# Kernel optimization log

Hardware: AMD Instinct MI355X
Metric: run time of the kernel (lower is better)

Reference implementation:

```python
import jax, jax.numpy as jnp
import numpy as np

DIM = 768
DEPTH = 6
HEADS = 12
DIM_HEAD = 64
INNER = HEADS * DIM_HEAD  # 768
MLP = DIM * 4
B, N = 4, 2048
EPS = 1e-5


def setup_inputs() -> dict:
    key = jax.random.key(0)
    ks = jax.random.split(key, 8)
    s = lambda *sh: 0.02
    inp = {
        "x": jax.random.normal(ks[0], (B, N, DIM), dtype=jnp.float32),
        "ln1_g": jnp.ones((DEPTH, DIM), jnp.float32),
        "ln1_b": jnp.zeros((DEPTH, DIM), jnp.float32),
        "wqkv": jax.random.normal(ks[1], (DEPTH, DIM, 3 * INNER), jnp.float32) * 0.02,
        "wout": jax.random.normal(ks[2], (DEPTH, INNER, DIM), jnp.float32) * 0.02,
        "ln2_g": jnp.ones((DEPTH, DIM), jnp.float32),
        "ln2_b": jnp.zeros((DEPTH, DIM), jnp.float32),
        "w1": jax.random.normal(ks[3], (DEPTH, DIM, MLP), jnp.float32) * 0.02,
        "b1": jnp.zeros((DEPTH, MLP), jnp.float32),
        "w2": jax.random.normal(ks[4], (DEPTH, MLP, DIM), jnp.float32) * 0.02,
        "b2": jnp.zeros((DEPTH, DIM), jnp.float32),
        "fn_g": jnp.ones((DIM,), jnp.float32),
        "fn_b": jnp.zeros((DIM,), jnp.float32),
    }
    return inp


def layer_norm(x, g, b):
    mu = jnp.mean(x, axis=-1, keepdims=True)
    var = jnp.mean(jnp.square(x - mu), axis=-1, keepdims=True)
    return (x - mu) * jax.lax.rsqrt(var + EPS) * g + b


def attention(x, wqkv, wout):
    # x: [b, n, dim]
    qkv = x @ wqkv  # [b, n, 3*inner]
    q, k, v = jnp.split(qkv, 3, axis=-1)
    split_heads = lambda t: t.reshape(t.shape[0], t.shape[1], HEADS, DIM_HEAD).transpose(0, 2, 1, 3)
    q, k, v = split_heads(q), split_heads(k), split_heads(v)  # [b, h, n, d]
    scale = DIM_HEAD ** -0.5
    dots = jnp.einsum("bhnd,bhmd->bhnm", q, k) * scale
    attn = jax.nn.softmax(dots, axis=-1)
    out = jnp.einsum("bhnm,bhmd->bhnd", attn, v)
    out = out.transpose(0, 2, 1, 3).reshape(x.shape[0], x.shape[1], INNER)
    return out @ wout


def feed_forward(x, w1, b1, w2, b2):
    h = jax.nn.gelu(x @ w1 + b1, approximate=False)
    return h @ w2 + b2


def reference(x, ln1_g, ln1_b, wqkv, wout, ln2_g, ln2_b, w1, b1, w2, b2, fn_g, fn_b):
    for i in range(DEPTH):
        x = x + attention(layer_norm(x, ln1_g[i], ln1_b[i]), wqkv[i], wout[i])
        x = x + feed_forward(layer_norm(x, ln2_g[i], ln2_b[i]), w1[i], b1[i], w2[i], b2[i])
    return layer_norm(x, fn_g, fn_b)
```

## Files before the change

### kernel.cpp

```cpp
#include <hip/hip_runtime.h>
#include <hip/hip_bf16.h>

typedef unsigned short ushort_t;
typedef unsigned int uint_t;
typedef __bf16 bf16x8 __attribute__((ext_vector_type(8)));
typedef float floatx4 __attribute__((ext_vector_type(4)));
typedef float floatx16 __attribute__((ext_vector_type(16)));

#define DIM 768
#define DEPTH 6
#define HEADS 12
#define DH 64
#define MLP_DIM 3072
#define BATCH 4
#define SEQ 2048
#define MTOK (BATCH * SEQ)
#define QKV3 (3 * DIM)

__device__ __forceinline__ float bf2f(unsigned u) {
    return __uint_as_float((u & 0xffffu) << 16);
}
__device__ __forceinline__ ushort_t f2bf(float f) {
    unsigned x = __float_as_uint(f);
    return (ushort_t)((x + 0x7FFFu + ((x >> 16) & 1u)) >> 16);
}
__device__ __forceinline__ void load_lds16(const void* g, void* l) {
    __builtin_amdgcn_global_load_lds((const __attribute__((address_space(1))) uint_t*)g,
                                     (__attribute__((address_space(3))) uint_t*)l, 16, 0, 0);
}
__device__ __forceinline__ uint_t cvt_pk_bf16(float lo, float hi) {
    uint_t r;
    asm("v_cvt_pk_bf16_f32 %0, %1, %2" : "=v"(r) : "v"(lo), "v"(hi));
    return r;
}
__device__ __forceinline__ float exp2_raw(float x) {
#if __has_builtin(__builtin_amdgcn_exp2f)
    return __builtin_amdgcn_exp2f(x);
#else
    return exp2f(x);
#endif
}

__global__ __launch_bounds__(256) void transpose_cvt(const float* __restrict__ in,
                                                     ushort_t* __restrict__ out,
                                                     int K, int N) {
    __shared__ float tile[32][33];
    const int d = blockIdx.z;
    in += (size_t)d * K * N;
    out += (size_t)d * K * N;
    const int n0 = blockIdx.x * 32, k0 = blockIdx.y * 32;
    for (int i = threadIdx.y; i < 32; i += 8) {
        tile[i][threadIdx.x] = in[(size_t)(k0 + i) * N + n0 + threadIdx.x];
    }
    __syncthreads();
    for (int i = threadIdx.y; i < 32; i += 8) {
        out[(size_t)(n0 + i) * K + k0 + threadIdx.x] = f2bf(tile[threadIdx.x][i]);
    }
}

template <bool OUTBF>
__global__ __launch_bounds__(256) void layernorm_k(const float* __restrict__ x,
                                                   const float* __restrict__ g,
                                                   const float* __restrict__ bta,
                                                   void* __restrict__ out) {
    const int row = blockIdx.x, t = threadIdx.x;
    const float* xr = x + (size_t)row * DIM;
    float v0 = xr[t], v1 = xr[t + 256], v2 = xr[t + 512];
    float s = v0 + v1 + v2;
    float sq = v0 * v0 + v1 * v1 + v2 * v2;
#pragma unroll
    for (int off = 32; off > 0; off >>= 1) {
        s += __shfl_down(s, off, 64);
        sq += __shfl_down(sq, off, 64);
    }
    __shared__ float ss[4], ssq[4];
    const int w = t >> 6;
    if ((t & 63) == 0) { ss[w] = s; ssq[w] = sq; }
    __syncthreads();
    s = ss[0] + ss[1] + ss[2] + ss[3];
    sq = ssq[0] + ssq[1] + ssq[2] + ssq[3];
    const float mean = s * (1.0f / DIM);
    const float var = sq * (1.0f / DIM) - mean * mean;
    const float rstd = rsqrtf(var + 1e-5f);
    float y0 = (v0 - mean) * rstd * g[t] + bta[t];
    float y1 = (v1 - mean) * rstd * g[t + 256] + bta[t + 256];
    float y2 = (v2 - mean) * rstd * g[t + 512] + bta[t + 512];
    if (OUTBF) {
        ushort_t* o = (ushort_t*)out + (size_t)row * DIM;
        o[t] = f2bf(y0); o[t + 256] = f2bf(y1); o[t + 512] = f2bf(y2);
    } else {
        float* o = (float*)out + (size_t)row * DIM;
        o[t] = y0; o[t + 256] = y1; o[t + 512] = y2;
    }
}

template <bool BIAS, bool GELU, bool RES, bool OUTBF>
__global__ __launch_bounds__(256) void gemm_bt(const ushort_t* __restrict__ A,
                                               const ushort_t* __restrict__ Bt,
                                               const float* __restrict__ bias,
                                               const float* __restrict__ resid,
                                               void* __restrict__ Cout,
                                               int M, int N, int K) {
    __shared__ ushort_t lds_a[2][128 * 32];
    __shared__ ushort_t lds_b[2][128 * 32];
    const int t = threadIdx.x;
    const int lane = t & 63, w = t >> 6;
    const int wm = w >> 1, wn = w & 1;

    const int nwg = gridDim.x * gridDim.y;
    int bid = blockIdx.y * gridDim.x + blockIdx.x;
    bid = (bid & 7) * (nwg >> 3) + (bid >> 3);
    const int bx = bid % gridDim.x, by = bid / gridDim.x;
    const int bm = by * 128, bn = bx * 128;

    floatx4 acc[4][4];
#pragma unroll
    for (int i = 0; i < 4; i++)
#pragma unroll
        for (int j = 0; j < 4; j++) acc[i][j] = (floatx4)0.0f;

    const int arow = t >> 2;
    const int asw = ((t & 3) ^ ((t >> 3) & 3)) * 8;
    const ushort_t* Abase = A + (size_t)(bm + arow) * K + asw;
    const ushort_t* Bbase = Bt + (size_t)(bn + arow) * K + asw;

    const int mrow = wm * 64 + (lane & 15);
    const int nrow = wn * 64 + (lane & 15);
    const int quad = lane >> 4;
    const int kca = (quad ^ ((mrow >> 1) & 3)) * 8;
    const int kcb = (quad ^ ((nrow >> 1) & 3)) * 8;

    const int nk = K >> 5;
    auto stage = [&](int kt) {
        const int bsel = kt & 1;
        const int k0 = kt * 32;
        ushort_t* la = lds_a[bsel] + t * 8;
        ushort_t* lb = lds_b[bsel] + t * 8;
        load_lds16(Abase + k0, la);
        load_lds16(Abase + (size_t)64 * K + k0, la + 64 * 32);
        load_lds16(Bbase + k0, lb);
        load_lds16(Bbase + (size_t)64 * K + k0, lb + 64 * 32);
    };

    stage(0);
    for (int kt = 0; kt < nk; kt++) {
        __syncthreads();
        if (kt + 1 < nk) stage(kt + 1);
        const ushort_t* la = lds_a[kt & 1];
        const ushort_t* lb = lds_b[kt & 1];

        bf16x8 af[4], bfr[4];
#pragma unroll
        for (int i = 0; i < 4; i++) {
            af[i] = *(const bf16x8*)(la + (mrow + i * 16) * 32 + kca);
            bfr[i] = *(const bf16x8*)(lb + (nrow + i * 16) * 32 + kcb);
        }
#pragma unroll
        for (int i = 0; i < 4; i++)
#pragma unroll
            for (int j = 0; j < 4; j++)
                acc[i][j] = __builtin_amdgcn_mfma_f32_16x16x32_bf16(af[i], bfr[j], acc[i][j], 0, 0, 0);
    }

    const int colq = lane & 15, rq = lane >> 4;
#pragma unroll
    for (int j = 0; j < 4; j++) {
        const int col = bn + wn * 64 + j * 16 + colq;
        const float bv = BIAS ? bias[col] : 0.0f;
#pragma unroll
        for (int i = 0; i < 4; i++) {
#pragma unroll
            for (int r = 0; r < 4; r++) {
                const int row = bm + wm * 64 + i * 16 + rq * 4 + r;
                float v = acc[i][j][r] + bv;
                if (GELU) v = 0.5f * v * (1.0f + erff(v * 0.70710678118654752f));
                const size_t idx = (size_t)row * N + col;
                if (RES) v += resid[idx];
                if (OUTBF) ((ushort_t*)Cout)[idx] = f2bf(v);
                else ((float*)Cout)[idx] = v;
            }
        }
    }
}

#define TSTR 66

__global__ __launch_bounds__(256) void v_transpose(const ushort_t* __restrict__ qkv,
                                                   ushort_t* __restrict__ vt) {
    __shared__ ushort_t tile[64 * TSTR];
    const int t = threadIdx.x;
    const int tk = blockIdx.x, h = blockIdx.y, b = blockIdx.z;
#pragma unroll
    for (int rep = 0; rep < 2; rep++) {
        const int s = t + rep * 256;
        const int row = s >> 3, uo = (s & 7) * 8;
        *(uint4*)(tile + row * TSTR + uo) =
            *(const uint4*)(qkv + (size_t)(b * SEQ + tk * 64 + row) * QKV3 + 2 * DIM + h * DH + uo);
    }
    __syncthreads();
#pragma unroll
    for (int rep = 0; rep < 2; rep++) {
        const int s = t + rep * 256;
        const int d = s >> 3, to = (s & 7) * 8;
        ushort_t tmp[8];
#pragma unroll
        for (int j = 0; j < 8; j++) tmp[j] = tile[(to + j) * TSTR + d];
        *(uint4*)(vt + ((size_t)(b * HEADS + h) * DH + d) * SEQ + tk * 64 + to) = *(uint4*)tmp;
    }
}

#define SC2 0.18033688011112042f

__global__ __launch_bounds__(256, 3) void attn_mfma(const ushort_t* __restrict__ qkv,
                                                    const ushort_t* __restrict__ vt,
                                                    ushort_t* __restrict__ outp) {
    __shared__ ushort_t lds_k[2][64 * 64];
    __shared__ ushort_t lds_vt[2][64 * 64];

    const int t = threadIdx.x;
    const int lane = t & 63, w = t >> 6;
    const int h = blockIdx.y, b = blockIdx.z;
    const int q0 = blockIdx.x * 128 + w * 32;
    const int l31 = lane & 31, hi = lane >> 5;

    bf16x8 qf[4];
#pragma unroll
    for (int dc = 0; dc < 4; dc++) {
        const uint4 raw = *(const uint4*)(qkv + (size_t)(b * SEQ + q0 + l31) * QKV3 +
                                          h * DH + dc * 16 + hi * 8);
        const uint_t rr[4] = {raw.x, raw.y, raw.z, raw.w};
        union { ushort_t u[8]; bf16x8 v; } qq;
#pragma unroll
        for (int e = 0; e < 4; e++) {
            qq.u[2 * e] = f2bf(bf2f(rr[e]) * SC2);
            qq.u[2 * e + 1] = f2bf(bf2f(rr[e] >> 16) * SC2);
        }
        qf[dc] = qq.v;
    }

    union { ushort_t u[8]; bf16x8 v; } onef;
#pragma unroll
    for (int e = 0; e < 8; e++) onef.u[e] = 0x3F80;

    floatx16 o[2];
    o[0] = (floatx16)0.0f; o[1] = (floatx16)0.0f;
    floatx16 osum = (floatx16)0.0f;

    const int srow = w * 16 + (lane >> 3);
    const int sg = ((lane & 7) ^ ((lane >> 3) & 7)) * 8;
    const ushort_t* kgbase = qkv + (size_t)(b * SEQ + srow) * QKV3 + DIM + h * DH + sg;
    const ushort_t* vgbase = vt + ((size_t)(b * HEADS + h) * DH + srow) * SEQ + sg;

    auto stage = [&](int kt) {
        const int bsel = kt & 1;
        ushort_t* ldk = (ushort_t*)lds_k[bsel] + w * 16 * 64;
        ushort_t* ldv = (ushort_t*)lds_vt[bsel] + w * 16 * 64;
        const ushort_t* kg = kgbase + (size_t)kt * 64 * QKV3;
        const ushort_t* vg = vgbase + kt * 64;
        load_lds16(kg, ldk);
        load_lds16(kg + (size_t)8 * QKV3, ldk + 8 * 64);
        load_lds16(vg, ldv);
        load_lds16(vg + (size_t)8 * SEQ, ldv + 8 * 64);
    };

    stage(0);
    for (int kt = 0; kt < SEQ / 64; kt++) {
        __syncthreads();
        stage((kt + 1) & (SEQ / 64 - 1));
        const ushort_t* ldk = lds_k[kt & 1];
        const ushort_t* ldv = lds_vt[kt & 1];

#pragma unroll
        for (int kt2 = 0; kt2 < 2; kt2++) {
            const int krow = kt2 * 32 + l31;
            const int ksw = krow & 7;
            floatx16 s = (floatx16)0.0f;
#pragma unroll
            for (int dc = 0; dc < 4; dc++) {
                const bf16x8 kf = *(const bf16x8*)(ldk + krow * 64 + ((dc * 2 + hi) ^ ksw) * 8);
                s = __builtin_amdgcn_mfma_f32_32x32x16_bf16(kf, qf[dc], s, 0, 0, 0);
            }

            bf16x8 vfr[2][2];
#pragma unroll
            for (int kc = 0; kc < 2; kc++)
#pragma unroll
                for (int dhalf = 0; dhalf < 2; dhalf++) {
                    const int vrow = dhalf * 32 + l31;
                    const int kcg = kt2 * 2 + kc;
                    vfr[kc][dhalf] =
                        *(const bf16x8*)(ldv + vrow * 64 + (((kcg * 2 + hi) ^ (vrow & 7)) * 8));
                }

            float p[16];
#pragma unroll
            for (int r = 0; r < 16; r++) p[r] = exp2_raw(s[r]);

#pragma unroll
            for (int kc = 0; kc < 2; kc++) {
                uint_t da = cvt_pk_bf16(p[kc * 8 + 0], p[kc * 8 + 1]);
                uint_t db = cvt_pk_bf16(p[kc * 8 + 2], p[kc * 8 + 3]);
                uint_t dcq = cvt_pk_bf16(p[kc * 8 + 4], p[kc * 8 + 5]);
                uint_t dd = cvt_pk_bf16(p[kc * 8 + 6], p[kc * 8 + 7]);
                asm volatile("v_permlane32_swap_b32 %0, %1" : "+v"(da), "+v"(dcq));
                asm volatile("v_permlane32_swap_b32 %0, %1" : "+v"(db), "+v"(dd));
                union { uint_t u[4]; bf16x8 v; } pa;
                pa.u[0] = da; pa.u[1] = db; pa.u[2] = dcq; pa.u[3] = dd;
                osum = __builtin_amdgcn_mfma_f32_32x32x16_bf16(pa.v, onef.v, osum, 0, 0, 0);
                o[0] = __builtin_amdgcn_mfma_f32_32x32x16_bf16(pa.v, vfr[kc][0], o[0], 0, 0, 0);
                o[1] = __builtin_amdgcn_mfma_f32_32x32x16_bf16(pa.v, vfr[kc][1], o[1], 0, 0, 0);
            }
        }
    }

#pragma unroll
    for (int r = 0; r < 16; r++) {
        const int ql = (r & 3) + 8 * (r >> 2) + 4 * hi;
        const float inv = 1.0f / osum[r];
        const size_t rowbase = (size_t)(b * SEQ + q0 + ql) * DIM + h * DH;
        outp[rowbase + l31] = f2bf(o[0][r] * inv);
        outp[rowbase + 32 + l31] = f2bf(o[1][r] * inv);
    }
}

extern "C" void kernel_launch(void* const* d_in, const int* in_sizes, int n_in,
                              void* d_out, int out_size, void* d_ws, size_t ws_size,
                              hipStream_t stream) {
    const float* x_in  = (const float*)d_in[0];
    const float* ln1_g = (const float*)d_in[1];
    const float* ln1_b = (const float*)d_in[2];
    const float* wqkv  = (const float*)d_in[3];
    const float* wout  = (const float*)d_in[4];
    const float* ln2_g = (const float*)d_in[5];
    const float* ln2_b = (const float*)d_in[6];
    const float* w1    = (const float*)d_in[7];
    const float* b1    = (const float*)d_in[8];
    const float* w2    = (const float*)d_in[9];
    const float* b2    = (const float*)d_in[10];
    const float* fn_g  = (const float*)d_in[11];
    const float* fn_b  = (const float*)d_in[12];

    char* ws = (char*)d_ws;
    size_t off = 0;
    auto alloc = [&](size_t bytes) -> char* {
        char* p = ws + off;
        off = (off + bytes + 255) & ~(size_t)255;
        return p;
    };
    ushort_t* wT_qkv = (ushort_t*)alloc((size_t)DEPTH * QKV3 * DIM * 2);
    ushort_t* wT_out = (ushort_t*)alloc((size_t)DEPTH * DIM * DIM * 2);
    ushort_t* wT_1   = (ushort_t*)alloc((size_t)DEPTH * MLP_DIM * DIM * 2);
    ushort_t* wT_2   = (ushort_t*)alloc((size_t)DEPTH * DIM * MLP_DIM * 2);
    float*    xbuf   = (float*)alloc((size_t)MTOK * DIM * 4);
    ushort_t* lnbuf  = (ushort_t*)alloc((size_t)MTOK * DIM * 2);
    ushort_t* qkvbuf = (ushort_t*)alloc((size_t)MTOK * QKV3 * 2);
    ushort_t* attnbuf= (ushort_t*)alloc((size_t)MTOK * DIM * 2);
    ushort_t* hbuf   = (ushort_t*)alloc((size_t)MTOK * MLP_DIM * 2);
    ushort_t* vtbuf  = hbuf;
    (void)ws_size; (void)in_sizes; (void)n_in; (void)out_size;

    transpose_cvt<<<dim3(QKV3 / 32, DIM / 32, DEPTH), dim3(32, 8), 0, stream>>>(wqkv, wT_qkv, DIM, QKV3);
    transpose_cvt<<<dim3(DIM / 32, DIM / 32, DEPTH), dim3(32, 8), 0, stream>>>(wout, wT_out, DIM, DIM);
    transpose_cvt<<<dim3(MLP_DIM / 32, DIM / 32, DEPTH), dim3(32, 8), 0, stream>>>(w1, wT_1, DIM, MLP_DIM);
    transpose_cvt<<<dim3(DIM / 32, MLP_DIM / 32, DEPTH), dim3(32, 8), 0, stream>>>(w2, wT_2, MLP_DIM, DIM);

    hipMemcpyAsync(xbuf, x_in, (size_t)MTOK * DIM * sizeof(float), hipMemcpyDeviceToDevice, stream);

    for (int i = 0; i < DEPTH; i++) {
        layernorm_k<true><<<MTOK, 256, 0, stream>>>(xbuf, ln1_g + i * DIM, ln1_b + i * DIM, lnbuf);
        gemm_bt<false, false, false, true><<<dim3(QKV3 / 128, MTOK / 128), 256, 0, stream>>>(
            lnbuf, wT_qkv + (size_t)i * QKV3 * DIM, nullptr, nullptr, qkvbuf, MTOK, QKV3, DIM);
        v_transpose<<<dim3(SEQ / 64, HEADS, BATCH), 256, 0, stream>>>(qkvbuf, vtbuf);
        attn_mfma<<<dim3(SEQ / 128, HEADS, BATCH), 256, 0, stream>>>(qkvbuf, vtbuf, attnbuf);
        gemm_bt<false, false, true, false><<<dim3(DIM / 128, MTOK / 128), 256, 0, stream>>>(
            attnbuf, wT_out + (size_t)i * DIM * DIM, nullptr, xbuf, xbuf, MTOK, DIM, DIM);
        layernorm_k<true><<<MTOK, 256, 0, stream>>>(xbuf, ln2_g + i * DIM, ln2_b + i * DIM, lnbuf);
        gemm_bt<true, true, false, true><<<dim3(MLP_DIM / 128, MTOK / 128), 256, 0, stream>>>(
            lnbuf, wT_1 + (size_t)i * MLP_DIM * DIM, b1 + (size_t)i * MLP_DIM, nullptr, hbuf, MTOK, MLP_DIM, DIM);
        gemm_bt<true, false, true, false><<<dim3(DIM / 128, MTOK / 128), 256, 0, stream>>>(
            hbuf, wT_2 + (size_t)i * DIM * MLP_DIM, b2 + (size_t)i * DIM, xbuf, xbuf, MTOK, DIM, MLP_DIM);
    }
    layernorm_k<false><<<MTOK, 256, 0, stream>>>(xbuf, fn_g, fn_b, (float*)d_out);
}
```

Before: 2.013 ms.

## Rewrite GEMM as 8-wave 128x256 tile with triple-buffered K=64 pipeline

Replaces the 4-wave 128x128 GEMM with a 512-thread kernel that computes 128x256 tiles, uses K-steps of 64 with an XOR swizzle over 8 chunks, and keeps three LDS buffers so that loads run two stages ahead. Explicit vmcnt waits replace the full __syncthreads wait. The goal is more global-load overlap and fewer barriers per unit of MFMA work. In exchange it uses 144KB of LDS per block, which limits occupancy to one block per CU. The larger tiles also produce fewer blocks for the N=768 GEMMs (3x64 grid), which may leave CUs underused.

Measured after the change: 1.931 ms. -4.1%, faster.

```diff
diff --git a/kernel.cpp b/kernel.cpp
--- a/kernel.cpp
+++ b/kernel.cpp
@@ -95,23 +95,22 @@
 }
 
 template <bool BIAS, bool GELU, bool RES, bool OUTBF>
-__global__ __launch_bounds__(256) void gemm_bt(const ushort_t* __restrict__ A,
-                                               const ushort_t* __restrict__ Bt,
-                                               const float* __restrict__ bias,
-                                               const float* __restrict__ resid,
-                                               void* __restrict__ Cout,
-                                               int M, int N, int K) {
-    __shared__ ushort_t lds_a[2][128 * 32];
-    __shared__ ushort_t lds_b[2][128 * 32];
+__global__ __launch_bounds__(512) void gemm8(const ushort_t* __restrict__ A,
+                                             const ushort_t* __restrict__ Bt,
+                                             const float* __restrict__ bias,
+                                             const float* __restrict__ resid,
+                                             void* __restrict__ Cout,
+                                             int M, int N, int K) {
+    __shared__ ushort_t lds[3 * 24576];
     const int t = threadIdx.x;
     const int lane = t & 63, w = t >> 6;
-    const int wm = w >> 1, wn = w & 1;
+    const int wm = w >> 2, wn = w & 3;
 
     const int nwg = gridDim.x * gridDim.y;
     int bid = blockIdx.y * gridDim.x + blockIdx.x;
     bid = (bid & 7) * (nwg >> 3) + (bid >> 3);
     const int bx = bid % gridDim.x, by = bid / gridDim.x;
-    const int bm = by * 128, bn = bx * 128;
+    const int bm = by * 128, bn = bx * 256;
 
     floatx4 acc[4][4];
 #pragma unroll
@@ -119,47 +118,55 @@
 #pragma unroll
         for (int j = 0; j < 4; j++) acc[i][j] = (floatx4)0.0f;
 
-    const int arow = t >> 2;
-    const int asw = ((t & 3) ^ ((t >> 3) & 3)) * 8;
-    const ushort_t* Abase = A + (size_t)(bm + arow) * K + asw;
-    const ushort_t* Bbase = Bt + (size_t)(bn + arow) * K + asw;
-
-    const int mrow = wm * 64 + (lane & 15);
-    const int nrow = wn * 64 + (lane & 15);
-    const int quad = lane >> 4;
-    const int kca = (quad ^ ((mrow >> 1) & 3)) * 8;
-    const int kcb = (quad ^ ((nrow >> 1) & 3)) * 8;
-
-    const int nk = K >> 5;
+    const int srow = t >> 3;
+    const int sw = ((t & 7) ^ ((t >> 3) & 7)) * 8;
+    const ushort_t* Ab = A + (size_t)(bm + srow) * K + sw;
+    const ushort_t* Bb = Bt + (size_t)(bn + srow) * K + sw;
+
+    const int nk = K >> 6;
     auto stage = [&](int kt) {
-        const int bsel = kt & 1;
-        const int k0 = kt * 32;
-        ushort_t* la = lds_a[bsel] + t * 8;
-        ushort_t* lb = lds_b[bsel] + t * 8;
-        load_lds16(Abase + k0, la);
-        load_lds16(Abase + (size_t)64 * K + k0, la + 64 * 32);
-        load_lds16(Bbase + k0, lb);
-        load_lds16(Bbase + (size_t)64 * K + k0, lb + 64 * 32);
+        ushort_t* ls = lds + (kt % 3) * 24576;
+        const int k0 = kt * 64;
+        load_lds16(Ab + k0, ls + t * 8);
+        load_lds16(Ab + (size_t)64 * K + k0, ls + 4096 + t * 8);
+        ushort_t* lb = ls + 8192;
+        load_lds16(Bb + k0, lb + t * 8);
+        load_lds16(Bb + (size_t)64 * K + k0, lb + 4096 + t * 8);
+        load_lds16(Bb + (size_t)128 * K + k0, lb + 8192 + t * 8);
+        load_lds16(Bb + (size_t)192 * K + k0, lb + 12288 + t * 8);
     };
 
     stage(0);
+    if (nk > 1) stage(1);
+
+    const int l15 = lane & 15, quad = lane >> 4;
+    const int arow = wm * 64 + l15;
+    const int brow = wn * 64 + l15;
+    const int swz = l15 & 7;
+
     for (int kt = 0; kt < nk; kt++) {
-        __syncthreads();
-        if (kt + 1 < nk) stage(kt + 1);
-        const ushort_t* la = lds_a[kt & 1];
-        const ushort_t* lb = lds_b[kt & 1];
-
-        bf16x8 af[4], bfr[4];
-#pragma unroll
-        for (int i = 0; i < 4; i++) {
-            af[i] = *(const bf16x8*)(la + (mrow + i * 16) * 32 + kca);
-            bfr[i] = *(const bf16x8*)(lb + (nrow + i * 16) * 32 + kcb);
+        if (kt < nk - 1) asm volatile("s_waitcnt vmcnt(6)" ::: "memory");
+        else             asm volatile("s_waitcnt vmcnt(0)" ::: "memory");
+        __builtin_amdgcn_s_barrier();
+        if (kt + 2 < nk) stage(kt + 2);
+        const ushort_t* Al = lds + (kt % 3) * 24576;
+        const ushort_t* Bl = Al + 8192;
+#pragma unroll
+        for (int ks = 0; ks < 2; ks++) {
+            const int kc = ((ks * 4 + quad) ^ swz) * 8;
+            bf16x8 af[4], bf[4];
+#pragma unroll
+            for (int i = 0; i < 4; i++)
+                af[i] = *(const bf16x8*)(Al + (arow + i * 16) * 64 + kc);
+#pragma unroll
+            for (int j = 0; j < 4; j++)
+                bf[j] = *(const bf16x8*)(Bl + (brow + j * 16) * 64 + kc);
+#pragma unroll
+            for (int i = 0; i < 4; i++)
+#pragma unroll
+                for (int j = 0; j < 4; j++)
+                    acc[i][j] = __builtin_amdgcn_mfma_f32_16x16x32_bf16(af[i], bf[j], acc[i][j], 0, 0, 0);
         }
-#pragma unroll
-        for (int i = 0; i < 4; i++)
-#pragma unroll
-            for (int j = 0; j < 4; j++)
-                acc[i][j] = __builtin_amdgcn_mfma_f32_16x16x32_bf16(af[i], bfr[j], acc[i][j], 0, 0, 0);
     }
 
     const int colq = lane & 15, rq = lane >> 4;
@@ -368,16 +375,16 @@
 
     for (int i = 0; i < DEPTH; i++) {
         layernorm_k<true><<<MTOK, 256, 0, stream>>>(xbuf, ln1_g + i * DIM, ln1_b + i * DIM, lnbuf);
-        gemm_bt<false, false, false, true><<<dim3(QKV3 / 128, MTOK / 128), 256, 0, stream>>>(
+        gemm8<false, false, false, true><<<dim3(QKV3 / 256, MTOK / 128), 512, 0, stream>>>(
             lnbuf, wT_qkv + (size_t)i * QKV3 * DIM, nullptr, nullptr, qkvbuf, MTOK, QKV3, DIM);
         v_transpose<<<dim3(SEQ / 64, HEADS, BATCH), 256, 0, stream>>>(qkvbuf, vtbuf);
         attn_mfma<<<dim3(SEQ / 128, HEADS, BATCH), 256, 0, stream>>>(qkvbuf, vtbuf, attnbuf);
-        gemm_bt<false, false, true, false><<<dim3(DIM / 128, MTOK / 128), 256, 0, stream>>>(
+        gemm8<false, false, true, false><<<dim3(DIM / 256, MTOK / 128), 512, 0, stream>>>(
             attnbuf, wT_out + (size_t)i * DIM * DIM, nullptr, xbuf, xbuf, MTOK, DIM, DIM);
         layernorm_k<true><<<MTOK, 256, 0, stream>>>(xbuf, ln2_g + i * DIM, ln2_b + i * DIM, lnbuf);
-        gemm_bt<true, true, false, true><<<dim3(MLP_DIM / 128, MTOK / 128), 256, 0, stream>>>(
+        gemm8<true, true, false, true><<<dim3(MLP_DIM / 256, MTOK / 128), 512, 0, stream>>>(
             lnbuf, wT_1 + (size_t)i * MLP_DIM * DIM, b1 + (size_t)i * MLP_DIM, nullptr, hbuf, MTOK, MLP_DIM, DIM);
-        gemm_bt<true, false, true, false><<<dim3(DIM / 128, MTOK / 128), 256, 0, stream>>>(
+        gemm8<true, false, true, false><<<dim3(DIM / 256, MTOK / 128), 512, 0, stream>>>(
             hbuf, wT_2 + (size_t)i * DIM * MLP_DIM, b2 + (size_t)i * DIM, xbuf, xbuf, MTOK, DIM, MLP_DIM);
     }
     layernorm_k<false><<<MTOK, 256, 0, stream>>>(xbuf, fn_g, fn_b, (float*)d_out);
```
